# Optimization experiments

Hardware: AMD Instinct MI355X
Metric: run time of the kernel (lower is better)

The kernel has to match this reference:

```python
import jax, jax.numpy as jnp
import numpy as np

NUM_FEATURES = 20480
NUM_ACC = 128
BATCH = 4096
SPARSITY_P = 0.0015  # ~30 active features per position, like real NNUE


def setup_inputs() -> dict:
    key = jax.random.key(0)
    kw, kb, k1, k2, k3, k4 = jax.random.split(key, 6)
    # sparse binary one-hot-per-piece feature vectors
    white = (jax.random.uniform(kw, (BATCH, NUM_FEATURES)) < SPARSITY_P).astype(jnp.float32)
    black = (jax.random.uniform(kb, (BATCH, NUM_FEATURES)) < SPARSITY_P).astype(jnp.float32)
    psqt_w = jax.random.normal(k1, (2, NUM_FEATURES), dtype=jnp.float32) * 0.02
    acc_w = jax.random.normal(k2, (NUM_ACC, NUM_FEATURES), dtype=jnp.float32) * 0.02
    acc_b = jax.random.normal(k3, (NUM_ACC,), dtype=jnp.float32) * 0.02
    out_w = jax.random.normal(k4, (2, NUM_ACC), dtype=jnp.float32) * 0.1
    return {"white": white, "black": black, "psqt_w": psqt_w,
            "acc_w": acc_w, "acc_b": acc_b, "out_w": out_w}


def _side(x, psqt_w, acc_w, acc_b, out_w):
    # psqt: [B,2]; accumulator: [B,128]; CReLU then Linear(128->2, no bias)
    psqt = x @ psqt_w.T                              # [B, 2]
    acc = jnp.clip(x @ acc_w.T + acc_b, 0.0, 1.0)    # [B, 128]
    pos = acc @ out_w.T                              # [B, 2]
    return psqt, pos


def reference(white, black, psqt_w, acc_w, acc_b, out_w):
    psqt_w_, pos_w = _side(white, psqt_w, acc_w, acc_b, out_w)
    psqt_b, pos_b = _side(black, psqt_w, acc_w, acc_b, out_w)
    return (psqt_w_ - psqt_b) + (pos_w - pos_b)      # [B, 2]
```

## Files before the change

### kernel.cpp

```cpp
#include <hip/hip_runtime.h>

#define NF   20480
#define NACC 128
#define BATCH 4096
#define MAXI 96

typedef unsigned int uvec4 __attribute__((ext_vector_type(4)));
typedef float        fvec4 __attribute__((ext_vector_type(4)));

__global__ __launch_bounds__(256) void transpose_accw(const float* __restrict__ acc_w,
                                                      float* __restrict__ accT) {
    __shared__ float tile[NACC][33];
    const int t  = threadIdx.x;
    const int f0 = blockIdx.x * 32;
    const int fl = t & 31;
    const int cr = t >> 5;
    #pragma unroll
    for (int i = 0; i < 16; ++i) {
        int cc = i * 8 + cr;
        tile[cc][fl] = acc_w[(size_t)cc * NF + f0 + fl];
    }
    __syncthreads();
    const int c  = t & 127;
    const int fr = t >> 7;
    #pragma unroll
    for (int i = 0; i < 16; ++i) {
        int ff = i * 2 + fr;
        accT[(size_t)(f0 + ff) * NACC + c] = tile[c][ff];
    }
}

#define PROCV(u, base)                                                          \
    if (u.x | u.y | u.z | u.w) {                                                \
        if (u.x) { int p = atomicAdd(cnt, 1); if (p < MAXI) idx[p] = (base) + 0; } \
        if (u.y) { int p = atomicAdd(cnt, 1); if (p < MAXI) idx[p] = (base) + 1; } \
        if (u.z) { int p = atomicAdd(cnt, 1); if (p < MAXI) idx[p] = (base) + 2; } \
        if (u.w) { int p = atomicAdd(cnt, 1); if (p < MAXI) idx[p] = (base) + 3; } \
    }

__global__ __launch_bounds__(256) void nnue_main(
    const float* __restrict__ white,
    const float* __restrict__ black,
    const float* __restrict__ psqt_w,
    const float* __restrict__ accT,
    const float* __restrict__ acc_b,
    const float* __restrict__ out_w,
    float* __restrict__ out)
{
    __shared__ int   s_cnt[2];
    __shared__ int   s_idx[2][MAXI];
    __shared__ fvec4 s_part[2][4][32];
    __shared__ float s_red[8];

    const int t    = threadIdx.x;
    const int b    = blockIdx.x;
    const int side = t >> 7;
    const int lt   = t & 127;

    const float bias = acc_b[lt];
    const float ow0  = out_w[lt];
    const float ow1  = out_w[NACC + lt];
    const float sgn  = side ? -1.f : 1.f;

    const float* X  = (side ? black : white) + (size_t)b * NF;
    const uvec4* Xv = (const uvec4*)X;

    if (t < 2) s_cnt[t] = 0;
    __syncthreads();

    int* cnt = &s_cnt[side];
    int* idx = s_idx[side];

    #pragma unroll 2
    for (int i = 0; i < 10; ++i) {
        const int v = i * 512 + lt;
        uvec4 a0 = __builtin_nontemporal_load(&Xv[v]);
        uvec4 a1 = __builtin_nontemporal_load(&Xv[v + 128]);
        uvec4 a2 = __builtin_nontemporal_load(&Xv[v + 256]);
        uvec4 a3 = __builtin_nontemporal_load(&Xv[v + 384]);
        if (a0.x|a0.y|a0.z|a0.w | a1.x|a1.y|a1.z|a1.w |
            a2.x|a2.y|a2.z|a2.w | a3.x|a3.y|a3.z|a3.w) {
            PROCV(a0, (v      ) * 4)
            PROCV(a1, (v + 128) * 4)
            PROCV(a2, (v + 256) * 4)
            PROCV(a3, (v + 384) * 4)
        }
    }
    __syncthreads();

    const int n      = min(s_cnt[side], MAXI);
    const int sub    = (t >> 5) & 3;
    const int lane32 = t & 31;
    const int* sIdx  = s_idx[side];

    float ps0 = 0.f, ps1 = 0.f;
    if (lt < n) {
        int f = sIdx[lt];
        ps0 = psqt_w[f];
        ps1 = psqt_w[NF + f];
    }

    fvec4 acc4 = {0.f, 0.f, 0.f, 0.f};
    for (int j = sub; j < n; j += 4) {
        int f = sIdx[j];
        acc4 += *(const fvec4*)&accT[(size_t)f * NACC + lane32 * 4];
    }
    s_part[side][sub][lane32] = acc4;
    __syncthreads();

    const float* sp = (const float*)&s_part[side][0][0];
    float a = sp[0 * NACC + lt] + sp[1 * NACC + lt]
            + sp[2 * NACC + lt] + sp[3 * NACC + lt];
    float h  = fminf(fmaxf(a + bias, 0.f), 1.f);
    float p0 = sgn * (h * ow0 + ps0);
    float p1 = sgn * (h * ow1 + ps1);

    #pragma unroll
    for (int off = 32; off > 0; off >>= 1) {
        p0 += __shfl_down(p0, off, 64);
        p1 += __shfl_down(p1, off, 64);
    }
    if ((t & 63) == 0) { int wv = t >> 6; s_red[wv * 2] = p0; s_red[wv * 2 + 1] = p1; }
    __syncthreads();

    if (t == 0) {
        out[(size_t)b * 2 + 0] = s_red[0] + s_red[2] + s_red[4] + s_red[6];
        out[(size_t)b * 2 + 1] = s_red[1] + s_red[3] + s_red[5] + s_red[7];
    }
}

extern "C" void kernel_launch(void* const* d_in, const int* in_sizes, int n_in,
                              void* d_out, int out_size, void* d_ws, size_t ws_size,
                              hipStream_t stream) {
    const float* white  = (const float*)d_in[0];
    const float* black  = (const float*)d_in[1];
    const float* psqt_w = (const float*)d_in[2];
    const float* acc_w  = (const float*)d_in[3];
    const float* acc_b  = (const float*)d_in[4];
    const float* out_w  = (const float*)d_in[5];
    float* out = (float*)d_out;

    float* accT = (float*)d_ws;

    transpose_accw<<<NF / 32, 256, 0, stream>>>(acc_w, accT);
    nnue_main<<<BATCH, 256, 0, stream>>>(white, black, psqt_w, accT,
                                         acc_b, out_w, out);
}
```

Measured before the change: 609.2 us.

## Process two batch rows per block with bf16 weight table and gather prefetch

Each block now handles two batch rows, prefetching the first row's weight gathers before scanning the second row so the gather latency overlaps the dense input scan. The transposed accumulator table is stored as bf16, halving gather bytes and table write traffic. The input scan loop is no longer unrolled. The bf16 rounding adds small numerical error, and the block count is halved, which may reduce latency hiding.

```diff
diff --git a/kernel.cpp b/kernel.cpp
--- a/kernel.cpp
+++ b/kernel.cpp
@@ -1,15 +1,29 @@
 #include <hip/hip_runtime.h>
 
-#define NF   20480
-#define NACC 128
+#define NF    20480
+#define NACC  128
 #define BATCH 4096
-#define MAXI 96
+#define MAXI  96
+#define PRE   8
 
 typedef unsigned int uvec4 __attribute__((ext_vector_type(4)));
+typedef unsigned int uvec2 __attribute__((ext_vector_type(2)));
 typedef float        fvec4 __attribute__((ext_vector_type(4)));
 
+__device__ __forceinline__ float bflo(unsigned int w) {
+    union { unsigned int u; float f; } v; v.u = w << 16; return v.f;
+}
+__device__ __forceinline__ float bfhi(unsigned int w) {
+    union { unsigned int u; float f; } v; v.u = w & 0xFFFF0000u; return v.f;
+}
+__device__ __forceinline__ unsigned short f2bf(float f) {
+    union { float f; unsigned int i; } v; v.f = f;
+    unsigned int x = v.i;
+    return (unsigned short)((x + 0x7FFFu + ((x >> 16) & 1u)) >> 16);
+}
+
 __global__ __launch_bounds__(256) void transpose_accw(const float* __restrict__ acc_w,
-                                                      float* __restrict__ accT) {
+                                                      unsigned short* __restrict__ accT) {
     __shared__ float tile[NACC][33];
     const int t  = threadIdx.x;
     const int f0 = blockIdx.x * 32;
@@ -26,52 +40,21 @@
     #pragma unroll
     for (int i = 0; i < 16; ++i) {
         int ff = i * 2 + fr;
-        accT[(size_t)(f0 + ff) * NACC + c] = tile[c][ff];
-    }
-}
-
-#define PROCV(u, base)                                                          \
-    if (u.x | u.y | u.z | u.w) {                                                \
+        accT[(size_t)(f0 + ff) * NACC + c] = f2bf(tile[c][ff]);
+    }
+}
+
+#define PROCV(u, base, cnt, idx)                                                   \
+    if (u.x | u.y | u.z | u.w) {                                                   \
         if (u.x) { int p = atomicAdd(cnt, 1); if (p < MAXI) idx[p] = (base) + 0; } \
         if (u.y) { int p = atomicAdd(cnt, 1); if (p < MAXI) idx[p] = (base) + 1; } \
         if (u.z) { int p = atomicAdd(cnt, 1); if (p < MAXI) idx[p] = (base) + 2; } \
         if (u.w) { int p = atomicAdd(cnt, 1); if (p < MAXI) idx[p] = (base) + 3; } \
     }
 
-__global__ __launch_bounds__(256) void nnue_main(
-    const float* __restrict__ white,
-    const float* __restrict__ black,
-    const float* __restrict__ psqt_w,
-    const float* __restrict__ accT,
-    const float* __restrict__ acc_b,
-    const float* __restrict__ out_w,
-    float* __restrict__ out)
-{
-    __shared__ int   s_cnt[2];
-    __shared__ int   s_idx[2][MAXI];
-    __shared__ fvec4 s_part[2][4][32];
-    __shared__ float s_red[8];
-
-    const int t    = threadIdx.x;
-    const int b    = blockIdx.x;
-    const int side = t >> 7;
-    const int lt   = t & 127;
-
-    const float bias = acc_b[lt];
-    const float ow0  = out_w[lt];
-    const float ow1  = out_w[NACC + lt];
-    const float sgn  = side ? -1.f : 1.f;
-
-    const float* X  = (side ? black : white) + (size_t)b * NF;
-    const uvec4* Xv = (const uvec4*)X;
-
-    if (t < 2) s_cnt[t] = 0;
-    __syncthreads();
-
-    int* cnt = &s_cnt[side];
-    int* idx = s_idx[side];
-
-    #pragma unroll 2
+__device__ __forceinline__ void scan_row(const uvec4* __restrict__ Xv, int lt,
+                                         int* cnt, int* idx) {
+    #pragma unroll 1
     for (int i = 0; i < 10; ++i) {
         const int v = i * 512 + lt;
         uvec4 a0 = __builtin_nontemporal_load(&Xv[v]);
@@ -80,52 +63,145 @@
         uvec4 a3 = __builtin_nontemporal_load(&Xv[v + 384]);
         if (a0.x|a0.y|a0.z|a0.w | a1.x|a1.y|a1.z|a1.w |
             a2.x|a2.y|a2.z|a2.w | a3.x|a3.y|a3.z|a3.w) {
-            PROCV(a0, (v      ) * 4)
-            PROCV(a1, (v + 128) * 4)
-            PROCV(a2, (v + 256) * 4)
-            PROCV(a3, (v + 384) * 4)
+            PROCV(a0, (v      ) * 4, cnt, idx)
+            PROCV(a1, (v + 128) * 4, cnt, idx)
+            PROCV(a2, (v + 256) * 4, cnt, idx)
+            PROCV(a3, (v + 384) * 4, cnt, idx)
         }
     }
-    __syncthreads();
-
-    const int n      = min(s_cnt[side], MAXI);
+}
+
+__global__ __launch_bounds__(256) void nnue_main(
+    const float* __restrict__ white,
+    const float* __restrict__ black,
+    const float* __restrict__ psqt_w,
+    const unsigned short* __restrict__ accT,
+    const float* __restrict__ acc_b,
+    const float* __restrict__ out_w,
+    float* __restrict__ out)
+{
+    __shared__ int   s_cnt[2][2];
+    __shared__ int   s_idx[2][2][MAXI];
+    __shared__ fvec4 s_part[2][4][32];
+    __shared__ float s_red[2][8];
+
+    const int t      = threadIdx.x;
+    const int side   = t >> 7;
+    const int lt     = t & 127;
     const int sub    = (t >> 5) & 3;
     const int lane32 = t & 31;
-    const int* sIdx  = s_idx[side];
-
+    const int b0     = blockIdx.x * 2;
+    const int b1     = b0 + 1;
+
+    const float bias = acc_b[lt];
+    const float ow0  = out_w[lt];
+    const float ow1  = out_w[NACC + lt];
+    const float sgn  = side ? -1.f : 1.f;
+
+    const float* base = side ? black : white;
+    const uvec4* Xv0 = (const uvec4*)(base + (size_t)b0 * NF);
+    const uvec4* Xv1 = (const uvec4*)(base + (size_t)b1 * NF);
+
+    if (t < 4) ((int*)s_cnt)[t] = 0;
+    __syncthreads();
+
+    scan_row(Xv0, lt, &s_cnt[0][side], s_idx[0][side]);
+    __syncthreads();
+
+    const int n0 = min(s_cnt[0][side], MAXI);
+
+    uvec2 pre[PRE];
+    unsigned mbits = 0;
+    #pragma unroll
+    for (int k = 0; k < PRE; ++k) {
+        int j = sub + 4 * k;
+        int f = (j < n0) ? s_idx[0][side][j] : 0;
+        mbits |= (j < n0) ? (1u << k) : 0u;
+        pre[k] = *(const uvec2*)(accT + (size_t)f * NACC + lane32 * 4);
+    }
     float ps0 = 0.f, ps1 = 0.f;
-    if (lt < n) {
-        int f = sIdx[lt];
+    if (lt < n0) {
+        int f = s_idx[0][side][lt];
         ps0 = psqt_w[f];
         ps1 = psqt_w[NF + f];
     }
 
-    fvec4 acc4 = {0.f, 0.f, 0.f, 0.f};
-    for (int j = sub; j < n; j += 4) {
-        int f = sIdx[j];
-        acc4 += *(const fvec4*)&accT[(size_t)f * NACC + lane32 * 4];
-    }
-    s_part[side][sub][lane32] = acc4;
+    scan_row(Xv1, lt, &s_cnt[1][side], s_idx[1][side]);
+    __syncthreads();
+
+    fvec4 acc0 = {0.f, 0.f, 0.f, 0.f};
+    #pragma unroll
+    for (int k = 0; k < PRE; ++k) {
+        float m = (float)((mbits >> k) & 1u);
+        uvec2 w = pre[k];
+        acc0.x += m * bflo(w.x); acc0.y += m * bfhi(w.x);
+        acc0.z += m * bflo(w.y); acc0.w += m * bfhi(w.y);
+    }
+    for (int j = 32 + sub; j < n0; j += 4) {
+        int f = s_idx[0][side][j];
+        uvec2 w = *(const uvec2*)(accT + (size_t)f * NACC + lane32 * 4);
+        acc0.x += bflo(w.x); acc0.y += bfhi(w.x);
+        acc0.z += bflo(w.y); acc0.w += bfhi(w.y);
+    }
+    s_part[side][sub][lane32] = acc0;
+
+    const int n1 = min(s_cnt[1][side], MAXI);
+    float ps0b = 0.f, ps1b = 0.f;
+    if (lt < n1) {
+        int f = s_idx[1][side][lt];
+        ps0b = psqt_w[f];
+        ps1b = psqt_w[NF + f];
+    }
+    fvec4 acc1 = {0.f, 0.f, 0.f, 0.f};
+    for (int j = sub; j < n1; j += 4) {
+        int f = s_idx[1][side][j];
+        uvec2 w = *(const uvec2*)(accT + (size_t)f * NACC + lane32 * 4);
+        acc1.x += bflo(w.x); acc1.y += bfhi(w.x);
+        acc1.z += bflo(w.y); acc1.w += bfhi(w.y);
+    }
     __syncthreads();
 
     const float* sp = (const float*)&s_part[side][0][0];
-    float a = sp[0 * NACC + lt] + sp[1 * NACC + lt]
-            + sp[2 * NACC + lt] + sp[3 * NACC + lt];
-    float h  = fminf(fmaxf(a + bias, 0.f), 1.f);
-    float p0 = sgn * (h * ow0 + ps0);
-    float p1 = sgn * (h * ow1 + ps1);
-
-    #pragma unroll
-    for (int off = 32; off > 0; off >>= 1) {
-        p0 += __shfl_down(p0, off, 64);
-        p1 += __shfl_down(p1, off, 64);
-    }
-    if ((t & 63) == 0) { int wv = t >> 6; s_red[wv * 2] = p0; s_red[wv * 2 + 1] = p1; }
-    __syncthreads();
-
+    {
+        float a = sp[0 * NACC + lt] + sp[1 * NACC + lt]
+                + sp[2 * NACC + lt] + sp[3 * NACC + lt];
+        float h  = fminf(fmaxf(a + bias, 0.f), 1.f);
+        float p0 = sgn * (h * ow0 + ps0);
+        float p1 = sgn * (h * ow1 + ps1);
+        #pragma unroll
+        for (int off = 32; off > 0; off >>= 1) {
+            p0 += __shfl_down(p0, off, 64);
+            p1 += __shfl_down(p1, off, 64);
+        }
+        if ((t & 63) == 0) { int wv = t >> 6; s_red[0][wv * 2] = p0; s_red[0][wv * 2 + 1] = p1; }
+    }
+    __syncthreads();
+
+    s_part[side][sub][lane32] = acc1;
     if (t == 0) {
-        out[(size_t)b * 2 + 0] = s_red[0] + s_red[2] + s_red[4] + s_red[6];
-        out[(size_t)b * 2 + 1] = s_red[1] + s_red[3] + s_red[5] + s_red[7];
+        out[(size_t)b0 * 2 + 0] = s_red[0][0] + s_red[0][2] + s_red[0][4] + s_red[0][6];
+        out[(size_t)b0 * 2 + 1] = s_red[0][1] + s_red[0][3] + s_red[0][5] + s_red[0][7];
+    }
+    __syncthreads();
+
+    {
+        float a = sp[0 * NACC + lt] + sp[1 * NACC + lt]
+                + sp[2 * NACC + lt] + sp[3 * NACC + lt];
+        float h  = fminf(fmaxf(a + bias, 0.f), 1.f);
+        float p0 = sgn * (h * ow0 + ps0b);
+        float p1 = sgn * (h * ow1 + ps1b);
+        #pragma unroll
+        for (int off = 32; off > 0; off >>= 1) {
+            p0 += __shfl_down(p0, off, 64);
+            p1 += __shfl_down(p1, off, 64);
+        }
+        if ((t & 63) == 0) { int wv = t >> 6; s_red[1][wv * 2] = p0; s_red[1][wv * 2 + 1] = p1; }
+    }
+    __syncthreads();
+
+    if (t == 0) {
+        out[(size_t)b1 * 2 + 0] = s_red[1][0] + s_red[1][2] + s_red[1][4] + s_red[1][6];
+        out[(size_t)b1 * 2 + 1] = s_red[1][1] + s_red[1][3] + s_red[1][5] + s_red[1][7];
     }
 }
 
@@ -140,9 +216,9 @@
     const float* out_w  = (const float*)d_in[5];
     float* out = (float*)d_out;
 
-    float* accT = (float*)d_ws;
+    unsigned short* accT = (unsigned short*)d_ws;
 
     transpose_accw<<<NF / 32, 256, 0, stream>>>(acc_w, accT);
-    nnue_main<<<BATCH, 256, 0, stream>>>(white, black, psqt_w, accT,
-                                         acc_b, out_w, out);
-}
+    nnue_main<<<BATCH / 2, 256, 0, stream>>>(white, black, psqt_w, accT,
+                                             acc_b, out_w, out);
+}
```

Result: no change. 610.9 us (+0.3%).
